# Performance work log

Hardware: AMD Instinct MI355X
Metric: run time of the kernel (lower is better)

The kernel has to match this reference:

```python
import jax, jax.numpy as jnp
import numpy as np

B, N_HIS, GRAPH_DIM, EMB, N_PRE = 32, 12, 307, 32, 12
DAY_STAMPS, WEEK_STATES = 288, 7
HID = EMB * N_PRE  # 384
STD, MEAN = 50.0, 60.0
LN_EPS = 1e-3  # keras LayerNormalization default epsilon


def setup_inputs() -> dict:
    key = jax.random.key(0)
    ks = jax.random.split(key, 32)
    gn = lambda k, shape, s: (jax.random.normal(k, shape, jnp.float32) * s)
    # inputs: [B, 1+n_his, 2+graph_dim]; row 0 carries (week, date) ids, rows 1: carry data
    x_data = gn(ks[0], (B, N_HIS, GRAPH_DIM), 1.0)
    week = jax.random.randint(ks[1], (B,), 0, WEEK_STATES)
    date = jax.random.randint(ks[2], (B,), 0, DAY_STAMPS)
    inputs = jnp.zeros((B, 1 + N_HIS, 2 + GRAPH_DIM), jnp.float32)
    inputs = inputs.at[:, 0, 0].set(week.astype(jnp.float32))
    inputs = inputs.at[:, 0, 1].set(date.astype(jnp.float32))
    inputs = inputs.at[:, 1:, 2:].set(x_data)
    d = {
        'inputs': inputs,
        'conv_w': gn(ks[3], (EMB,), 0.5),        # 1x1 Conv2D on 1 input channel
        'conv_b': gn(ks[4], (EMB,), 0.1),
        'dws': gn(ks[5], (DAY_STAMPS, N_HIS, EMB, EMB, N_HIS), (2.0 / (EMB * N_HIS)) ** 0.5),
        'dbs': gn(ks[6], (DAY_STAMPS, GRAPH_DIM, EMB, N_HIS), 0.02),
        'ln_gamma': jnp.ones((N_HIS,), jnp.float32),
        'ln_beta': jnp.zeros((N_HIS,), jnp.float32),
        'tge2tg': gn(ks[7], (GRAPH_DIM, EMB, GRAPH_DIM), (1.0 / (GRAPH_DIM * EMB)) ** 0.5),
        'gte2gt': gn(ks[8], (N_HIS, EMB, N_HIS), (1.0 / (N_HIS * EMB)) ** 0.5),
        'fully_w': gn(ks[9], (2 * N_HIS, N_PRE), (1.0 / (2 * N_HIS)) ** 0.5),
    }
    shapes = [(N_HIS, HID), (HID,), (HID, HID), (HID,), (HID, HID), (HID,), (HID, N_PRE), (N_PRE,)]
    names = ['w0', 'b0', 'w1', 'b1', 'w2', 'b2', 'w3', 'b3']
    ki = 10
    for pre in ('se_', 'te_'):
        for nm, sh in zip(names, shapes):
            s = 0.0 if nm.startswith('b') else (2.0 / sum(sh)) ** 0.5
            d[pre + nm] = gn(ks[ki], sh, s) if s > 0 else jnp.zeros(sh, jnp.float32)
            ki += 1
    return d


def _mlp(x, w0, b0, w1, b1, w2, b2, w3, b3):
    # MLP(layer_num=2): Dense(relu) -> Dense -> Dense(relu) -> Dense
    x = jax.nn.relu(x @ w0 + b0) @ w1 + b1
    x = jax.nn.relu(x @ w2 + b2) @ w3 + b3
    return x


def _forward(inputs, conv_w, conv_b, dws, dbs, ln_gamma, ln_beta,
             se_p, te_p, tge2tg, gte2gt, fully_w, date):
    x3 = inputs[:, 1:, 2:]                         # [B, t, g]
    xe = x3[..., None] * conv_w + conv_b           # 1x1 conv -> [B, t, g, e]
    xe = jnp.transpose(xe, (0, 2, 3, 1))           # [B, g, e, t]  ('bget')
    # talinear (dilation=False, week_flag=True): gather per-date weights, batched einsum
    dw = dws[date]                                 # [B, t, e, e, t']  ('bteij')
    db = dbs[date]                                 # [B, g, e, t']
    x = jnp.einsum('bget,bteij->bgij', xe, dw) + db
    # LayerNorm over last axis (n_his), keras default eps=1e-3
    m = jnp.mean(x, axis=-1, keepdims=True)
    v = jnp.var(x, axis=-1, keepdims=True)
    x = (x - m) * jax.lax.rsqrt(v + LN_EPS) * ln_gamma + ln_beta
    x = jnp.where(x >= 0, x, 0.3 * x)              # LeakyReLU(alpha=0.3); dropout inactive at inference
    xe2 = jnp.transpose(x, (0, 3, 1, 2))           # [B, t, g, e]
    tge = xe2
    gte = xe2.reshape(xe2.shape[0], GRAPH_DIM, N_HIS, EMB)  # faithful raw reshape (not transpose)
    x3t = jnp.transpose(x3, (0, 2, 1))             # [B, g, t]
    x1 = _mlp(x3t, *se_p)                          # [B, g, n_pre]
    x2 = _mlp(x3t, *te_p)
    tg = jnp.einsum('gev,btge->btv', tge2tg, tge)  # [B, t, g]
    tg2gt = jnp.transpose(tg, (0, 2, 1))           # [B, g, t]
    gt1 = (tg2gt + x1) * jax.nn.sigmoid(tg2gt)
    gt = jnp.einsum('teo,bgte->bgo', gte2gt, gte)  # [B, g, t]
    gt2 = (gt + x2) * jax.nn.sigmoid(gt)
    out = jnp.concatenate([gt1, gt2], axis=-1) @ fully_w  # [B, g, n_pre]
    out = jnp.transpose(out, (0, 2, 1)) * STD + MEAN      # z_inverse
    return out


def reference(inputs, conv_w, conv_b, dws, dbs, ln_gamma, ln_beta,
              se_w0, se_b0, se_w1, se_b1, se_w2, se_b2, se_w3, se_b3,
              te_w0, te_b0, te_w1, te_b1, te_w2, te_b2, te_w3, te_b3,
              tge2tg, gte2gt, fully_w):
    date = inputs[:, 0, 1].astype(jnp.int32)
    se_p = (se_w0, se_b0, se_w1, se_b1, se_w2, se_b2, se_w3, se_b3)
    te_p = (te_w0, te_b0, te_w1, te_b1, te_w2, te_b2, te_w3, te_b3)
    return _forward(inputs, conv_w, conv_b, dws, dbs, ln_gamma, ln_beta,
                    se_p, te_p, tge2tg, gte2gt, fully_w, date)
```

## Files before the change

kernel.cpp:

```cpp
#include <hip/hip_runtime.h>
#include <hip/hip_bf16.h>

#define NB   32
#define GDIM 307
#define IN_ROW 309
#define IN_B  (13*309)
#define NROWS (NB*GDIM)
#define MPAD  9856

typedef __attribute__((ext_vector_type(8))) short bf16x8;
typedef __attribute__((ext_vector_type(4))) float f32x4;

__device__ __forceinline__ void async_copy16(const void* g, void* l) {
  __builtin_amdgcn_global_load_lds(
      (const __attribute__((address_space(1))) void*)g,
      (__attribute__((address_space(3))) void*)l, 16, 0, 0);
}

__device__ __forceinline__ void mgemm_body(
    const __hip_bfloat16* __restrict__ A, int ldA,
    const __hip_bfloat16* __restrict__ Bt, int ldB,
    const float* bias, void* C, int ldC, long Czoff,
    int M, int N, int kt0, int kt1, int act, int outbf,
    char* smem, int m0, int n0) {
  const int tid = threadIdx.x;
  const int w = tid >> 6, lane = tid & 63;
  f32x4 acc[4][2];
  #pragma unroll
  for (int i=0;i<4;i++)
    #pragma unroll
    for (int j=0;j<2;j++) acc[i][j] = (f32x4){0.f,0.f,0.f,0.f};
  const int wm = (w>>1)*64, wn = (w&1)*32;
  const int l15 = lane & 15, lhi = lane >> 4;

  for (int kt = kt0; kt < kt1; ++kt) {
    const int k0 = kt*64;
    #pragma unroll
    for (int i=0;i<4;i++) {
      int c = w*256 + i*64 + lane;
      int row = c >> 3, j = c & 7;
      int jg = j ^ (row & 7);
      async_copy16(A + (size_t)(m0+row)*ldA + k0 + jg*8, smem + (w*256 + i*64)*16);
    }
    #pragma unroll
    for (int i=0;i<2;i++) {
      int c = w*128 + i*64 + lane;
      int row = c >> 3, j = c & 7;
      int jg = j ^ (row & 7);
      async_copy16(Bt + (size_t)(n0+row)*ldB + k0 + jg*8, smem + 16384 + (w*128 + i*64)*16);
    }
    __syncthreads();
    #pragma unroll
    for (int kk=0;kk<2;kk++) {
      bf16x8 af[4], bfr[2];
      #pragma unroll
      for (int fi=0; fi<4; fi++) {
        int row = wm + fi*16 + l15;
        af[fi] = *(const bf16x8*)(smem + row*128 + (((kk<<2)+lhi) ^ (row&7))*16);
      }
      #pragma unroll
      for (int fj=0; fj<2; fj++) {
        int n = wn + fj*16 + l15;
        bfr[fj] = *(const bf16x8*)(smem + 16384 + n*128 + (((kk<<2)+lhi) ^ (n&7))*16);
      }
      #pragma unroll
      for (int fi=0;fi<4;fi++)
        #pragma unroll
        for (int fj=0;fj<2;fj++)
          acc[fi][fj] = __builtin_amdgcn_mfma_f32_16x16x32_bf16(af[fi], bfr[fj], acc[fi][fj], 0, 0, 0);
    }
    __syncthreads();
  }

  #pragma unroll
  for (int fi=0;fi<4;fi++) {
    int row0 = m0 + wm + fi*16 + lhi*4;
    #pragma unroll
    for (int fj=0;fj<2;fj++) {
      int col = n0 + wn + fj*16 + l15;
      if (col < N) {
        float bv = bias ? bias[col] : 0.f;
        #pragma unroll
        for (int r=0;r<4;r++) {
          int row = row0 + r;
          if (row < M) {
            float v = acc[fi][fj][r] + bv;
            if (act) v = fmaxf(v, 0.f);
            if (outbf)
              ((__hip_bfloat16*)C)[(size_t)row*ldC + col] = __float2bfloat16(v);
            else
              ((float*)C + Czoff)[(size_t)row*ldC + col] = v;
          }
        }
      }
    }
  }
}

__global__ __launch_bounds__(256) void k_f1(
    const float* __restrict__ inp, const float* __restrict__ dws,
    const float* __restrict__ cw, const float* __restrict__ cb,
    float* __restrict__ A_pre, float* __restrict__ Cp,
    const float* se1, const float* se2, const float* te1, const float* te2,
    const float* se3, const float* te3, const float* g2g, const float* tgw,
    __hip_bfloat16* Wse1, __hip_bfloat16* Wse2, __hip_bfloat16* Wte1, __hip_bfloat16* Wte2,
    __hip_bfloat16* Wse3, __hip_bfloat16* Wte3, __hip_bfloat16* Wgt, __hip_bfloat16* Wtg,
    const float* se0, const float* seb0, const float* te0, const float* teb0,
    __hip_bfloat16* __restrict__ hA_se, __hip_bfloat16* __restrict__ hA_te) {
  __shared__ char smem[23040];
  int bid = blockIdx.x, tid = threadIdx.x;
  if (bid < 932) {
    float (*t)[65] = (float(*)[65])smem;
    const float* src; __hip_bfloat16* dst; int sK, sN, dR, ldD, bx, by;
    if (bid < 144) {
      int q = bid / 36, s = bid % 36; bx = s % 6; by = s / 6;
      src = q==0?se1 : q==1?se2 : q==2?te1 : te2;
      dst = q==0?Wse1: q==1?Wse2: q==2?Wte1: Wte2;
      sK = 384; sN = 384; dR = 384; ldD = 384;
    } else if (bid < 162) {
      int q = (bid-144)/6, s = (bid-144)%6; bx = s; by = 0;
      src = q==0?se3:q==1?te3:g2g;
      dst = q==0?Wse3:q==1?Wte3:Wgt;
      sK = 384; sN = 12; dR = 64; ldD = 384;
    } else {
      int s = bid - 162; bx = s % 154; by = s / 154;
      src = tgw; dst = Wtg; sK = 9824; sN = 307; dR = 320; ldD = 9856;
    }
    int k0 = bx*64, n0 = by*64;
    int tx = tid & 63, ty = tid >> 6;
    for (int r = ty; r < 64; r += 4) {
      int k = k0 + r, n = n0 + tx;
      t[r][tx] = (k < sK && n < sN) ? src[(size_t)k*sN + n] : 0.f;
    }
    __syncthreads();
    for (int r = ty; r < 64; r += 4) {
      int n = n0 + r, k = k0 + tx;
      if (n < dR && k < ldD) dst[(size_t)n*ldD + k] = __float2bfloat16(t[tx][r]);
    }
  } else if (bid < 1240) {
    int idx = bid - 932;
    int z = idx / 154, mt = idx - z*154;
    int r0 = mt*64;
    const float* w0 = z ? te0 : se0;
    const float* b0 = z ? teb0 : seb0;
    __hip_bfloat16* H = z ? hA_te : hA_se;
    float* sw = (float*)smem;
    float* sb = sw + 4608;
    float* sx = sb + 384;
    for (int i = tid; i < 4608; i += 256) sw[i] = w0[i];
    for (int i = tid; i < 384; i += 256) sb[i] = b0[i];
    for (int v = tid; v < 768; v += 256) {
      int r = v / 12, t = v - r*12;
      int row = r0 + r;
      float xv = 0.f;
      if (row < NROWS) {
        int b = row / GDIM, g = row - b*GDIM;
        xv = inp[b*IN_B + (1+t)*IN_ROW + 2 + g];
      }
      sx[v] = xv;
    }
    __syncthreads();
    for (int c = tid; c < 384; c += 256) {
      float wv[12];
      #pragma unroll
      for (int t = 0; t < 12; t++) wv[t] = sw[t*384 + c];
      float bv = sb[c];
      for (int r = 0; r < 64; r++) {
        int row = r0 + r;
        if (row >= NROWS) break;
        float acc = bv;
        #pragma unroll
        for (int t = 0; t < 12; t++) acc += sx[r*12+t] * wv[t];
        H[(size_t)row*384 + c] = __float2bfloat16(fmaxf(acc, 0.f));
      }
    }
  } else {
    int idx = bid - 1240;
    int b = idx / 12, t = idx - b*12;
    float* scw = (float*)smem;
    float* scb = scw + 32;
    if (tid < 32) { scw[tid] = cw[tid]; scb[tid] = cb[tid]; }
    __syncthreads();
    int date = (int)inp[b*IN_B + 1];
    const float* dw = dws + (size_t)date * 147456 + t*12288;
    for (int r = tid; r < 384; r += 256) {
      float sA = 0.f, sC = 0.f;
      #pragma unroll
      for (int e = 0; e < 32; e++) {
        float v = dw[e*384 + r];
        sA += scw[e] * v;
        sC += scb[e] * v;
      }
      A_pre[(b*12 + t)*384 + r] = sA;
      Cp[(b*12 + t)*384 + r]    = sC;
    }
  }
}

__global__ __launch_bounds__(256) void k_f2(
    const __hip_bfloat16* __restrict__ hA_se, const __hip_bfloat16* __restrict__ hA_te,
    const __hip_bfloat16* __restrict__ Wse1, const __hip_bfloat16* __restrict__ Wte1,
    const float* __restrict__ seb1, const float* __restrict__ teb1,
    __hip_bfloat16* __restrict__ hB_se, __hip_bfloat16* __restrict__ hB_te,
    const float* __restrict__ inp, const float* __restrict__ dbs,
    const float* __restrict__ A_pre, const float* __restrict__ Cp,
    const float* __restrict__ gamma, const float* __restrict__ beta,
    __hip_bfloat16* __restrict__ xlnT, __hip_bfloat16* __restrict__ xg) {
  __shared__ char smem[32640];
  int bid = blockIdx.x, tid = threadIdx.x;
  if (bid < 924) {
    int z = bid / 462, rem = bid - z*462;
    int n0 = (rem % 6)*64, m0 = (rem / 6)*128;
    mgemm_body(z ? hA_te : hA_se, 384, z ? Wte1 : Wse1, 384,
               z ? teb1 : seb1, z ? hB_te : hB_se, 384, 0,
               NROWS, 384, 0, 6, 0, 1, smem, m0, n0);
  } else {
    int idx = bid - 924;
    int b = idx / 39, gc = idx - b*39;
    int g0 = gc*8, ng = min(8, GDIM - g0);
    float* sA  = (float*)smem;
    float* sxb = sA + 4608;
    float* sCs = sxb + 3072;
    float* sx3 = sCs + 384;
    int date = (int)inp[b*IN_B + 1];
    for (int v = tid; v < 4608; v += 256) sA[v] = A_pre[b*4608 + v];
    for (int e = tid; e < 384; e += 256) {
      float s = 0.f;
      #pragma unroll
      for (int t = 0; t < 12; t++) s += Cp[b*4608 + t*384 + e];
      sCs[e] = s;
    }
    if (tid < ng*12) {
      int gl = tid / 12, t = tid - gl*12;
      sx3[tid] = inp[b*IN_B + (1+t)*IN_ROW + 2 + g0 + gl];
    }
    if (gc == 38) {
      for (int v = tid; v < 384; v += 256) {
        int j = v >> 5, c = v & 31;
        xlnT[(size_t)(b*12+j)*9856 + 9824 + c] = __float2bfloat16(0.f);
      }
    }
    __syncthreads();
    for (int o = tid; o < ng*384; o += 256) {
      int gl = o / 384, e = o - gl*384;
      float acc = sCs[e] + dbs[(size_t)date*117888 + (g0+gl)*384 + e];
      #pragma unroll
      for (int t = 0; t < 12; t++) acc += sx3[gl*12+t] * sA[t*384 + e];
      sxb[gl*384 + e] = acc;
    }
    __syncthreads();
    if (tid < ng*32) {
      int gl = tid >> 5, i = tid & 31;
      const float* xb = sxb + gl*384 + i*12;
      float m = 0.f;
      #pragma unroll
      for (int q = 0; q < 12; q++) m += xb[q];
      m *= (1.f/12.f);
      float v = 0.f;
      #pragma unroll
      for (int q = 0; q < 12; q++) { float d = xb[q] - m; v += d*d; }
      v *= (1.f/12.f);
      float rs = rsqrtf(v + 1e-3f);
      int g = g0 + gl;
      #pragma unroll
      for (int j = 0; j < 12; j++) {
        float y = (xb[j] - m) * rs * gamma[j] + beta[j];
        y = (y >= 0.f) ? y : 0.3f*y;
        __hip_bfloat16 yb = __float2bfloat16(y);
        xlnT[(size_t)(b*12 + j)*9856 + g*32 + i] = yb;
        int q2 = j*GDIM + g;
        int gq = q2 / 12, tq = q2 - gq*12;
        xg[(size_t)(b*GDIM + gq)*384 + tq*32 + i] = yb;
      }
    }
  }
}

__global__ __launch_bounds__(256) void k_f3(
    const __hip_bfloat16* __restrict__ hB_se, const __hip_bfloat16* __restrict__ hB_te,
    const __hip_bfloat16* __restrict__ Wse2, const __hip_bfloat16* __restrict__ Wte2,
    const float* __restrict__ seb2, const float* __restrict__ teb2,
    __hip_bfloat16* __restrict__ hA_se, __hip_bfloat16* __restrict__ hA_te,
    const __hip_bfloat16* __restrict__ xlnT, const __hip_bfloat16* __restrict__ Wtg,
    float* __restrict__ tgp,
    const __hip_bfloat16* __restrict__ xg, const __hip_bfloat16* __restrict__ Wgt,
    float* __restrict__ gtv) {
  __shared__ char smem[24576];
  int bid = blockIdx.x;
  if (bid < 924) {
    int z = bid / 462, rem = bid - z*462;
    int n0 = (rem % 6)*64, m0 = (rem / 6)*128;
    mgemm_body(z ? hB_te : hB_se, 384, z ? Wte2 : Wse2, 384,
               z ? teb2 : seb2, z ? hA_te : hA_se, 384, 0,
               NROWS, 384, 0, 6, 1, 1, smem, m0, n0);
  } else if (bid < 1164) {
    int idx = bid - 924;
    int z = idx / 15, rem = idx - z*15;
    int n0 = (rem % 5)*64, m0 = (rem / 5)*128;
    int kt0 = z*10, kt1 = min(154, kt0 + 10);
    mgemm_body(xlnT, 9856, Wtg, 9856, nullptr, tgp, 320, (long)z*122880,
               384, 320, kt0, kt1, 0, 0, smem, m0, n0);
  } else {
    int m0 = (bid - 1164)*128;
    mgemm_body(xg, 384, Wgt, 384, nullptr, gtv, 12, 0,
               NROWS, 12, 0, 6, 0, 0, smem, m0, 0);
  }
}

__global__ __launch_bounds__(256) void k_f4(
    const __hip_bfloat16* __restrict__ hA_se, const __hip_bfloat16* __restrict__ hA_te,
    const __hip_bfloat16* __restrict__ Wse3, const __hip_bfloat16* __restrict__ Wte3,
    const float* __restrict__ seb3, const float* __restrict__ teb3,
    float* __restrict__ x1, float* __restrict__ x2,
    const float* __restrict__ tgp, float* __restrict__ tgv) {
  __shared__ char smem[24576];
  int bid = blockIdx.x;
  if (bid < 154) {
    int z = bid / 77, m0 = (bid - z*77)*128;
    mgemm_body(z ? hA_te : hA_se, 384, z ? Wte3 : Wse3, 384,
               z ? teb3 : seb3, z ? x2 : x1, 12, 0,
               NROWS, 12, 0, 6, 0, 0, smem, m0, 0);
  } else {
    int base = (bid - 154) * 1024;
    #pragma unroll
    for (int q = 0; q < 4; q++) {
      int gid = base + q*256 + threadIdx.x;
      float s = 0.f;
      #pragma unroll
      for (int z = 0; z < 16; z++) s += tgp[(size_t)z*122880 + gid];
      tgv[gid] = s;
    }
  }
}

__global__ __launch_bounds__(256) void k_final(const float* __restrict__ tgv,
    const float* __restrict__ gt, const float* __restrict__ x1,
    const float* __restrict__ x2, const float* __restrict__ fw,
    float* __restrict__ out) {
  __shared__ float w[288];
  for (int idx = threadIdx.x; idx < 288; idx += 256) w[idx] = fw[idx];
  __syncthreads();
  int gid = blockIdx.x*256 + threadIdx.x;
  if (gid >= NROWS) return;
  int b = gid / GDIM, g = gid - b*GDIM;
  float g1[12], g2[12];
  #pragma unroll
  for (int n = 0; n < 12; n++) {
    float tv  = tgv[(size_t)(b*12+n)*320 + g];
    float x1v = x1[(size_t)gid*12 + n];
    float gv  = gt[(size_t)gid*12 + n];
    float x2v = x2[(size_t)gid*12 + n];
    float s1 = 1.f/(1.f + __expf(-tv));
    float s2 = 1.f/(1.f + __expf(-gv));
    g1[n] = (tv + x1v)*s1;
    g2[n] = (gv + x2v)*s2;
  }
  #pragma unroll
  for (int o = 0; o < 12; o++) {
    float acc = 0.f;
    #pragma unroll
    for (int n = 0; n < 12; n++)
      acc += g1[n]*w[n*12+o] + g2[n]*w[(12+n)*12+o];
    out[(size_t)(b*12+o)*GDIM + g] = acc*50.f + 60.f;
  }
}

extern "C" void kernel_launch(void* const* d_in, const int* in_sizes, int n_in,
                              void* d_out, int out_size, void* d_ws, size_t ws_size,
                              hipStream_t stream) {
  const float* inp    = (const float*)d_in[0];
  const float* cw     = (const float*)d_in[1];
  const float* cb     = (const float*)d_in[2];
  const float* dws    = (const float*)d_in[3];
  const float* dbs    = (const float*)d_in[4];
  const float* ln_g   = (const float*)d_in[5];
  const float* ln_b   = (const float*)d_in[6];
  const float* tge2tg = (const float*)d_in[7];
  const float* gte2gt = (const float*)d_in[8];
  const float* fullyw = (const float*)d_in[9];
  const float* se[8];
  const float* te[8];
  for (int i = 0; i < 8; i++) { se[i] = (const float*)d_in[10+i]; te[i] = (const float*)d_in[18+i]; }
  float* out = (float*)d_out;

  char* base = (char*)d_ws;
  size_t off = 0;
  auto alloc = [&](size_t bytes) { char* r = base + off; off += (bytes + 255) & ~(size_t)255; return r; };
  float* A_pre = (float*)alloc(147456*4);
  float* Cp    = (float*)alloc(147456*4);
  float* x1    = (float*)alloc(117888*4);
  float* x2    = (float*)alloc(117888*4);
  float* gtv   = (float*)alloc(117888*4);
  float* tgv   = (float*)alloc(122880*4);
  float* tgp   = (float*)alloc((size_t)16*122880*4);
  __hip_bfloat16* hA_se = (__hip_bfloat16*)alloc((size_t)MPAD*384*2);
  __hip_bfloat16* hA_te = (__hip_bfloat16*)alloc((size_t)MPAD*384*2);
  __hip_bfloat16* hB_se = (__hip_bfloat16*)alloc((size_t)MPAD*384*2);
  __hip_bfloat16* hB_te = (__hip_bfloat16*)alloc((size_t)MPAD*384*2);
  __hip_bfloat16* xlnT  = (__hip_bfloat16*)alloc((size_t)384*9856*2);
  __hip_bfloat16* xg    = (__hip_bfloat16*)alloc((size_t)MPAD*384*2);
  __hip_bfloat16* Wse1 = (__hip_bfloat16*)alloc(147456*2);
  __hip_bfloat16* Wse2 = (__hip_bfloat16*)alloc(147456*2);
  __hip_bfloat16* Wte1 = (__hip_bfloat16*)alloc(147456*2);
  __hip_bfloat16* Wte2 = (__hip_bfloat16*)alloc(147456*2);
  __hip_bfloat16* Wse3 = (__hip_bfloat16*)alloc(24576*2);
  __hip_bfloat16* Wte3 = (__hip_bfloat16*)alloc(24576*2);
  __hip_bfloat16* Wgt  = (__hip_bfloat16*)alloc(24576*2);
  __hip_bfloat16* Wtg  = (__hip_bfloat16*)alloc((size_t)320*9856*2);

  k_f1<<<1624, 256, 0, stream>>>(inp, dws, cw, cb, A_pre, Cp,
      se[2], se[4], te[2], te[4], se[6], te[6], gte2gt, tge2tg,
      Wse1, Wse2, Wte1, Wte2, Wse3, Wte3, Wgt, Wtg,
      se[0], se[1], te[0], te[1], hA_se, hA_te);

  k_f2<<<2172, 256, 0, stream>>>(hA_se, hA_te, Wse1, Wte1, se[3], te[3],
      hB_se, hB_te, inp, dbs, A_pre, Cp, ln_g, ln_b, xlnT, xg);

  k_f3<<<1241, 256, 0, stream>>>(hB_se, hB_te, Wse2, Wte2, se[5], te[5],
      hA_se, hA_te, xlnT, Wtg, tgp, xg, Wgt, gtv);

  k_f4<<<274, 256, 0, stream>>>(hA_se, hA_te, Wse3, Wte3, se[7], te[7], x1, x2, tgp, tgv);

  k_final<<<39, 256, 0, stream>>>(tgv, gtv, x1, x2, fullyw, out);
}
```

Measured before the change: 112.3 us.

## Fuse final MLP layer, split-K reduction and output gating into one kernel

Merges the last MLP GEMM, the split-K reduction of the tg partials and the final gating/projection into a single 512-thread kernel. The x1/x2 results now stay in LDS and never round-trip through global memory. The tg split-K count drops from 16 to 8 so each block covers more K, and block orderings are changed so the long-running tg GEMM and Wtg transpose blocks are dispatched first. This removes one launch and several intermediate buffers, but leaves only 77 blocks for the final stage and each thread sums 8 partials inline.

```diff
diff --git a/kernel.cpp b/kernel.cpp
--- a/kernel.cpp
+++ b/kernel.cpp
@@ -11,6 +11,15 @@
 typedef __attribute__((ext_vector_type(8))) short bf16x8;
 typedef __attribute__((ext_vector_type(4))) float f32x4;
 
+struct KP {
+  const float *inp,*dws,*cw,*cb,*dbs,*ln_g,*ln_b,*g2g,*tgw,*fw;
+  const float *se0,*seb0,*sew1,*seb1,*sew2,*seb2,*sew3,*seb3;
+  const float *te0,*teb0,*tew1,*teb1,*tew2,*teb2,*tew3,*teb3;
+  float *A_pre,*Cp,*gtv,*tgp,*out;
+  __hip_bfloat16 *hA_se,*hA_te,*hB_se,*hB_te,*xlnT,*xg;
+  __hip_bfloat16 *Wse1,*Wse2,*Wte1,*Wte2,*Wse3,*Wte3,*Wgt,*Wtg;
+};
+
 __device__ __forceinline__ void async_copy16(const void* g, void* l) {
   __builtin_amdgcn_global_load_lds(
       (const __attribute__((address_space(1))) void*)g,
@@ -21,9 +30,8 @@
     const __hip_bfloat16* __restrict__ A, int ldA,
     const __hip_bfloat16* __restrict__ Bt, int ldB,
     const float* bias, void* C, int ldC, long Czoff,
-    int M, int N, int kt0, int kt1, int act, int outbf,
-    char* smem, int m0, int n0) {
-  const int tid = threadIdx.x;
+    int M, int N, int kt0, int kt1, int act, int mode,
+    char* smem, int m0, int n0, float* ldsOut, int tid) {
   const int w = tid >> 6, lane = tid & 63;
   f32x4 acc[4][2];
   #pragma unroll
@@ -72,6 +80,22 @@
     __syncthreads();
   }
 
+  if (mode == 2) {
+    #pragma unroll
+    for (int fi=0;fi<4;fi++) {
+      int rl0 = wm + fi*16 + lhi*4;
+      #pragma unroll
+      for (int fj=0;fj<2;fj++) {
+        int col = wn + fj*16 + l15;
+        if (col < N) {
+          float bv = bias ? bias[col] : 0.f;
+          #pragma unroll
+          for (int r=0;r<4;r++) ldsOut[(rl0+r)*13 + col] = acc[fi][fj][r] + bv;
+        }
+      }
+    }
+    return;
+  }
   #pragma unroll
   for (int fi=0;fi<4;fi++) {
     int row0 = m0 + wm + fi*16 + lhi*4;
@@ -86,7 +110,7 @@
           if (row < M) {
             float v = acc[fi][fj][r] + bv;
             if (act) v = fmaxf(v, 0.f);
-            if (outbf)
+            if (mode == 1)
               ((__hip_bfloat16*)C)[(size_t)row*ldC + col] = __float2bfloat16(v);
             else
               ((float*)C + Czoff)[(size_t)row*ldC + col] = v;
@@ -97,34 +121,45 @@
   }
 }
 
-__global__ __launch_bounds__(256) void k_f1(
-    const float* __restrict__ inp, const float* __restrict__ dws,
-    const float* __restrict__ cw, const float* __restrict__ cb,
-    float* __restrict__ A_pre, float* __restrict__ Cp,
-    const float* se1, const float* se2, const float* te1, const float* te2,
-    const float* se3, const float* te3, const float* g2g, const float* tgw,
-    __hip_bfloat16* Wse1, __hip_bfloat16* Wse2, __hip_bfloat16* Wte1, __hip_bfloat16* Wte2,
-    __hip_bfloat16* Wse3, __hip_bfloat16* Wte3, __hip_bfloat16* Wgt, __hip_bfloat16* Wtg,
-    const float* se0, const float* seb0, const float* te0, const float* teb0,
-    __hip_bfloat16* __restrict__ hA_se, __hip_bfloat16* __restrict__ hA_te) {
-  __shared__ char smem[23040];
+__global__ __launch_bounds__(256) void k_p1(KP P) {
+  __shared__ alignas(16) char smem[23040];
   int bid = blockIdx.x, tid = threadIdx.x;
-  if (bid < 932) {
+  if (bid < 384) {
+    int b = bid / 12, t = bid - b*12;
+    float* scw = (float*)smem;
+    float* scb = scw + 32;
+    if (tid < 32) { scw[tid] = P.cw[tid]; scb[tid] = P.cb[tid]; }
+    __syncthreads();
+    int date = (int)P.inp[b*IN_B + 1];
+    const float* dw = P.dws + (size_t)date * 147456 + t*12288;
+    for (int r = tid; r < 384; r += 256) {
+      float sA = 0.f, sC = 0.f;
+      #pragma unroll
+      for (int e = 0; e < 32; e++) {
+        float v = dw[e*384 + r];
+        sA += scw[e] * v;
+        sC += scb[e] * v;
+      }
+      P.A_pre[(b*12 + t)*384 + r] = sA;
+      P.Cp[(b*12 + t)*384 + r]    = sC;
+    }
+  } else if (bid < 1316) {
     float (*t)[65] = (float(*)[65])smem;
+    int s = bid - 384;
     const float* src; __hip_bfloat16* dst; int sK, sN, dR, ldD, bx, by;
-    if (bid < 144) {
-      int q = bid / 36, s = bid % 36; bx = s % 6; by = s / 6;
-      src = q==0?se1 : q==1?se2 : q==2?te1 : te2;
-      dst = q==0?Wse1: q==1?Wse2: q==2?Wte1: Wte2;
+    if (s < 770) {
+      bx = s % 154; by = s / 154;
+      src = P.tgw; dst = P.Wtg; sK = 9824; sN = 307; dR = 320; ldD = 9856;
+    } else if (s < 914) {
+      int q = (s-770) / 36, u = (s-770) % 36; bx = u % 6; by = u / 6;
+      src = q==0?P.sew1 : q==1?P.sew2 : q==2?P.tew1 : P.tew2;
+      dst = q==0?P.Wse1 : q==1?P.Wse2 : q==2?P.Wte1 : P.Wte2;
       sK = 384; sN = 384; dR = 384; ldD = 384;
-    } else if (bid < 162) {
-      int q = (bid-144)/6, s = (bid-144)%6; bx = s; by = 0;
-      src = q==0?se3:q==1?te3:g2g;
-      dst = q==0?Wse3:q==1?Wte3:Wgt;
+    } else {
+      int q = (s-914) / 6, u = (s-914) % 6; bx = u; by = 0;
+      src = q==0?P.sew3 : q==1?P.tew3 : P.g2g;
+      dst = q==0?P.Wse3 : q==1?P.Wte3 : P.Wgt;
       sK = 384; sN = 12; dR = 64; ldD = 384;
-    } else {
-      int s = bid - 162; bx = s % 154; by = s / 154;
-      src = tgw; dst = Wtg; sK = 9824; sN = 307; dR = 320; ldD = 9856;
     }
     int k0 = bx*64, n0 = by*64;
     int tx = tid & 63, ty = tid >> 6;
@@ -137,13 +172,13 @@
       int n = n0 + r, k = k0 + tx;
       if (n < dR && k < ldD) dst[(size_t)n*ldD + k] = __float2bfloat16(t[tx][r]);
     }
-  } else if (bid < 1240) {
-    int idx = bid - 932;
+  } else {
+    int idx = bid - 1316;
     int z = idx / 154, mt = idx - z*154;
     int r0 = mt*64;
-    const float* w0 = z ? te0 : se0;
-    const float* b0 = z ? teb0 : seb0;
-    __hip_bfloat16* H = z ? hA_te : hA_se;
+    const float* w0 = z ? P.te0 : P.se0;
+    const float* b0 = z ? P.teb0 : P.seb0;
+    __hip_bfloat16* H = z ? P.hA_te : P.hA_se;
     float* sw = (float*)smem;
     float* sb = sw + 4608;
     float* sx = sb + 384;
@@ -155,7 +190,7 @@
       float xv = 0.f;
       if (row < NROWS) {
         int b = row / GDIM, g = row - b*GDIM;
-        xv = inp[b*IN_B + (1+t)*IN_ROW + 2 + g];
+        xv = P.inp[b*IN_B + (1+t)*IN_ROW + 2 + g];
       }
       sx[v] = xv;
     }
@@ -174,46 +209,17 @@
         H[(size_t)row*384 + c] = __float2bfloat16(fmaxf(acc, 0.f));
       }
     }
-  } else {
-    int idx = bid - 1240;
-    int b = idx / 12, t = idx - b*12;
-    float* scw = (float*)smem;
-    float* scb = scw + 32;
-    if (tid < 32) { scw[tid] = cw[tid]; scb[tid] = cb[tid]; }
-    __syncthreads();
-    int date = (int)inp[b*IN_B + 1];
-    const float* dw = dws + (size_t)date * 147456 + t*12288;
-    for (int r = tid; r < 384; r += 256) {
-      float sA = 0.f, sC = 0.f;
-      #pragma unroll
-      for (int e = 0; e < 32; e++) {
-        float v = dw[e*384 + r];
-        sA += scw[e] * v;
-        sC += scb[e] * v;
-      }
-      A_pre[(b*12 + t)*384 + r] = sA;
-      Cp[(b*12 + t)*384 + r]    = sC;
-    }
-  }
-}
-
-__global__ __launch_bounds__(256) void k_f2(
-    const __hip_bfloat16* __restrict__ hA_se, const __hip_bfloat16* __restrict__ hA_te,
-    const __hip_bfloat16* __restrict__ Wse1, const __hip_bfloat16* __restrict__ Wte1,
-    const float* __restrict__ seb1, const float* __restrict__ teb1,
-    __hip_bfloat16* __restrict__ hB_se, __hip_bfloat16* __restrict__ hB_te,
-    const float* __restrict__ inp, const float* __restrict__ dbs,
-    const float* __restrict__ A_pre, const float* __restrict__ Cp,
-    const float* __restrict__ gamma, const float* __restrict__ beta,
-    __hip_bfloat16* __restrict__ xlnT, __hip_bfloat16* __restrict__ xg) {
-  __shared__ char smem[32640];
+  }
+}
+
+__global__ __launch_bounds__(256) void k_p2(KP P) {
+  __shared__ alignas(16) char smem[32640];
   int bid = blockIdx.x, tid = threadIdx.x;
   if (bid < 924) {
     int z = bid / 462, rem = bid - z*462;
-    int n0 = (rem % 6)*64, m0 = (rem / 6)*128;
-    mgemm_body(z ? hA_te : hA_se, 384, z ? Wte1 : Wse1, 384,
-               z ? teb1 : seb1, z ? hB_te : hB_se, 384, 0,
-               NROWS, 384, 0, 6, 0, 1, smem, m0, n0);
+    mgemm_body(z ? P.hA_te : P.hA_se, 384, z ? P.Wte1 : P.Wse1, 384,
+               z ? P.teb1 : P.seb1, z ? P.hB_te : P.hB_se, 384, 0,
+               NROWS, 384, 0, 6, 0, 1, smem, (rem/6)*128, (rem%6)*64, nullptr, tid);
   } else {
     int idx = bid - 924;
     int b = idx / 39, gc = idx - b*39;
@@ -222,28 +228,28 @@
     float* sxb = sA + 4608;
     float* sCs = sxb + 3072;
     float* sx3 = sCs + 384;
-    int date = (int)inp[b*IN_B + 1];
-    for (int v = tid; v < 4608; v += 256) sA[v] = A_pre[b*4608 + v];
+    int date = (int)P.inp[b*IN_B + 1];
+    for (int v = tid; v < 4608; v += 256) sA[v] = P.A_pre[b*4608 + v];
     for (int e = tid; e < 384; e += 256) {
       float s = 0.f;
       #pragma unroll
-      for (int t = 0; t < 12; t++) s += Cp[b*4608 + t*384 + e];
+      for (int t = 0; t < 12; t++) s += P.Cp[b*4608 + t*384 + e];
       sCs[e] = s;
     }
     if (tid < ng*12) {
       int gl = tid / 12, t = tid - gl*12;
-      sx3[tid] = inp[b*IN_B + (1+t)*IN_ROW + 2 + g0 + gl];
+      sx3[tid] = P.inp[b*IN_B + (1+t)*IN_ROW + 2 + g0 + gl];
     }
     if (gc == 38) {
       for (int v = tid; v < 384; v += 256) {
         int j = v >> 5, c = v & 31;
-        xlnT[(size_t)(b*12+j)*9856 + 9824 + c] = __float2bfloat16(0.f);
+        P.xlnT[(size_t)(b*12+j)*9856 + 9824 + c] = __float2bfloat16(0.f);
       }
     }
     __syncthreads();
     for (int o = tid; o < ng*384; o += 256) {
       int gl = o / 384, e = o - gl*384;
-      float acc = sCs[e] + dbs[(size_t)date*117888 + (g0+gl)*384 + e];
+      float acc = sCs[e] + P.dbs[(size_t)date*117888 + (g0+gl)*384 + e];
       #pragma unroll
       for (int t = 0; t < 12; t++) acc += sx3[gl*12+t] * sA[t*384 + e];
       sxb[gl*384 + e] = acc;
@@ -264,162 +270,131 @@
       int g = g0 + gl;
       #pragma unroll
       for (int j = 0; j < 12; j++) {
-        float y = (xb[j] - m) * rs * gamma[j] + beta[j];
+        float y = (xb[j] - m) * rs * P.ln_g[j] + P.ln_b[j];
         y = (y >= 0.f) ? y : 0.3f*y;
         __hip_bfloat16 yb = __float2bfloat16(y);
-        xlnT[(size_t)(b*12 + j)*9856 + g*32 + i] = yb;
+        P.xlnT[(size_t)(b*12 + j)*9856 + g*32 + i] = yb;
         int q2 = j*GDIM + g;
         int gq = q2 / 12, tq = q2 - gq*12;
-        xg[(size_t)(b*GDIM + gq)*384 + tq*32 + i] = yb;
-      }
-    }
-  }
-}
-
-__global__ __launch_bounds__(256) void k_f3(
-    const __hip_bfloat16* __restrict__ hB_se, const __hip_bfloat16* __restrict__ hB_te,
-    const __hip_bfloat16* __restrict__ Wse2, const __hip_bfloat16* __restrict__ Wte2,
-    const float* __restrict__ seb2, const float* __restrict__ teb2,
-    __hip_bfloat16* __restrict__ hA_se, __hip_bfloat16* __restrict__ hA_te,
-    const __hip_bfloat16* __restrict__ xlnT, const __hip_bfloat16* __restrict__ Wtg,
-    float* __restrict__ tgp,
-    const __hip_bfloat16* __restrict__ xg, const __hip_bfloat16* __restrict__ Wgt,
-    float* __restrict__ gtv) {
-  __shared__ char smem[24576];
-  int bid = blockIdx.x;
-  if (bid < 924) {
-    int z = bid / 462, rem = bid - z*462;
-    int n0 = (rem % 6)*64, m0 = (rem / 6)*128;
-    mgemm_body(z ? hB_te : hB_se, 384, z ? Wte2 : Wse2, 384,
-               z ? teb2 : seb2, z ? hA_te : hA_se, 384, 0,
-               NROWS, 384, 0, 6, 1, 1, smem, m0, n0);
-  } else if (bid < 1164) {
-    int idx = bid - 924;
-    int z = idx / 15, rem = idx - z*15;
-    int n0 = (rem % 5)*64, m0 = (rem / 5)*128;
-    int kt0 = z*10, kt1 = min(154, kt0 + 10);
-    mgemm_body(xlnT, 9856, Wtg, 9856, nullptr, tgp, 320, (long)z*122880,
-               384, 320, kt0, kt1, 0, 0, smem, m0, n0);
+        P.xg[(size_t)(b*GDIM + gq)*384 + tq*32 + i] = yb;
+      }
+    }
+  }
+}
+
+__global__ __launch_bounds__(256) void k_p3(KP P) {
+  __shared__ alignas(16) char smem[24576];
+  int bid = blockIdx.x, tid = threadIdx.x;
+  if (bid < 120) {
+    int z = bid / 15, rem = bid - z*15;
+    int kt0 = z*20, kt1 = min(154, kt0 + 20);
+    mgemm_body(P.xlnT, 9856, P.Wtg, 9856, nullptr, P.tgp, 320, (long)z*122880,
+               384, 320, kt0, kt1, 0, 0, smem, (rem/5)*128, (rem%5)*64, nullptr, tid);
+  } else if (bid < 1044) {
+    int idx = bid - 120;
+    int z = idx / 462, rem = idx - z*462;
+    mgemm_body(z ? P.hB_te : P.hB_se, 384, z ? P.Wte2 : P.Wse2, 384,
+               z ? P.teb2 : P.seb2, z ? P.hA_te : P.hA_se, 384, 0,
+               NROWS, 384, 0, 6, 1, 1, smem, (rem/6)*128, (rem%6)*64, nullptr, tid);
   } else {
-    int m0 = (bid - 1164)*128;
-    mgemm_body(xg, 384, Wgt, 384, nullptr, gtv, 12, 0,
-               NROWS, 12, 0, 6, 0, 0, smem, m0, 0);
-  }
-}
-
-__global__ __launch_bounds__(256) void k_f4(
-    const __hip_bfloat16* __restrict__ hA_se, const __hip_bfloat16* __restrict__ hA_te,
-    const __hip_bfloat16* __restrict__ Wse3, const __hip_bfloat16* __restrict__ Wte3,
-    const float* __restrict__ seb3, const float* __restrict__ teb3,
-    float* __restrict__ x1, float* __restrict__ x2,
-    const float* __restrict__ tgp, float* __restrict__ tgv) {
-  __shared__ char smem[24576];
-  int bid = blockIdx.x;
-  if (bid < 154) {
-    int z = bid / 77, m0 = (bid - z*77)*128;
-    mgemm_body(z ? hA_te : hA_se, 384, z ? Wte3 : Wse3, 384,
-               z ? teb3 : seb3, z ? x2 : x1, 12, 0,
-               NROWS, 12, 0, 6, 0, 0, smem, m0, 0);
-  } else {
-    int base = (bid - 154) * 1024;
-    #pragma unroll
-    for (int q = 0; q < 4; q++) {
-      int gid = base + q*256 + threadIdx.x;
-      float s = 0.f;
-      #pragma unroll
-      for (int z = 0; z < 16; z++) s += tgp[(size_t)z*122880 + gid];
-      tgv[gid] = s;
-    }
-  }
-}
-
-__global__ __launch_bounds__(256) void k_final(const float* __restrict__ tgv,
-    const float* __restrict__ gt, const float* __restrict__ x1,
-    const float* __restrict__ x2, const float* __restrict__ fw,
-    float* __restrict__ out) {
-  __shared__ float w[288];
-  for (int idx = threadIdx.x; idx < 288; idx += 256) w[idx] = fw[idx];
+    int m0 = (bid - 1044)*128;
+    mgemm_body(P.xg, 384, P.Wgt, 384, nullptr, P.gtv, 12, 0,
+               NROWS, 12, 0, 6, 0, 0, smem, m0, 0, nullptr, tid);
+  }
+}
+
+__global__ __launch_bounds__(512) void k_p4(KP P) {
+  __shared__ alignas(16) char smem[63616];
+  float* x1s = (float*)(smem + 49152);
+  float* x2s = x1s + 1664;
+  float* fws = x2s + 1664;
+  int tid = threadIdx.x;
+  int half = tid >> 8, lt = tid & 255;
+  int r0 = blockIdx.x * 128;
+  for (int i = tid; i < 288; i += 512) fws[i] = P.fw[i];
+  mgemm_body(half ? P.hA_te : P.hA_se, 384, half ? P.Wte3 : P.Wse3, 384,
+             half ? P.teb3 : P.seb3, nullptr, 0, 0, NROWS, 12, 0, 6, 0, 2,
+             smem + half*24576, r0, 0, half ? x2s : x1s, lt);
   __syncthreads();
-  int gid = blockIdx.x*256 + threadIdx.x;
-  if (gid >= NROWS) return;
-  int b = gid / GDIM, g = gid - b*GDIM;
-  float g1[12], g2[12];
-  #pragma unroll
-  for (int n = 0; n < 12; n++) {
-    float tv  = tgv[(size_t)(b*12+n)*320 + g];
-    float x1v = x1[(size_t)gid*12 + n];
-    float gv  = gt[(size_t)gid*12 + n];
-    float x2v = x2[(size_t)gid*12 + n];
-    float s1 = 1.f/(1.f + __expf(-tv));
-    float s2 = 1.f/(1.f + __expf(-gv));
-    g1[n] = (tv + x1v)*s1;
-    g2[n] = (gv + x2v)*s2;
-  }
-  #pragma unroll
-  for (int o = 0; o < 12; o++) {
-    float acc = 0.f;
-    #pragma unroll
-    for (int n = 0; n < 12; n++)
-      acc += g1[n]*w[n*12+o] + g2[n]*w[(12+n)*12+o];
-    out[(size_t)(b*12+o)*GDIM + g] = acc*50.f + 60.f;
+  if (tid < 128) {
+    int row = r0 + tid;
+    if (row < NROWS) {
+      int b = row / GDIM, g = row - b*GDIM;
+      float g1[12], g2[12];
+      #pragma unroll
+      for (int n = 0; n < 12; n++) {
+        float tv = 0.f;
+        #pragma unroll
+        for (int z = 0; z < 8; z++) tv += P.tgp[(size_t)z*122880 + (b*12+n)*320 + g];
+        float gv  = P.gtv[(size_t)row*12 + n];
+        float x1v = x1s[tid*13 + n];
+        float x2v = x2s[tid*13 + n];
+        float s1 = 1.f/(1.f + __expf(-tv));
+        float s2 = 1.f/(1.f + __expf(-gv));
+        g1[n] = (tv + x1v)*s1;
+        g2[n] = (gv + x2v)*s2;
+      }
+      #pragma unroll
+      for (int o = 0; o < 12; o++) {
+        float a = 0.f;
+        #pragma unroll
+        for (int n = 0; n < 12; n++)
+          a += g1[n]*fws[n*12+o] + g2[n]*fws[(12+n)*12+o];
+        P.out[(size_t)(b*12+o)*GDIM + g] = a*50.f + 60.f;
+      }
+    }
   }
 }
 
 extern "C" void kernel_launch(void* const* d_in, const int* in_sizes, int n_in,
                               void* d_out, int out_size, void* d_ws, size_t ws_size,
                               hipStream_t stream) {
-  const float* inp    = (const float*)d_in[0];
-  const float* cw     = (const float*)d_in[1];
-  const float* cb     = (const float*)d_in[2];
-  const float* dws    = (const float*)d_in[3];
-  const float* dbs    = (const float*)d_in[4];
-  const float* ln_g   = (const float*)d_in[5];
-  const float* ln_b   = (const float*)d_in[6];
-  const float* tge2tg = (const float*)d_in[7];
-  const float* gte2gt = (const float*)d_in[8];
-  const float* fullyw = (const float*)d_in[9];
   const float* se[8];
   const float* te[8];
   for (int i = 0; i < 8; i++) { se[i] = (const float*)d_in[10+i]; te[i] = (const float*)d_in[18+i]; }
-  float* out = (float*)d_out;
 
   char* base = (char*)d_ws;
   size_t off = 0;
   auto alloc = [&](size_t bytes) { char* r = base + off; off += (bytes + 255) & ~(size_t)255; return r; };
-  float* A_pre = (float*)alloc(147456*4);
-  float* Cp    = (float*)alloc(147456*4);
-  float* x1    = (float*)alloc(117888*4);
-  float* x2    = (float*)alloc(117888*4);
-  float* gtv   = (float*)alloc(117888*4);
-  float* tgv   = (float*)alloc(122880*4);
-  float* tgp   = (float*)alloc((size_t)16*122880*4);
-  __hip_bfloat16* hA_se = (__hip_bfloat16*)alloc((size_t)MPAD*384*2);
-  __hip_bfloat16* hA_te = (__hip_bfloat16*)alloc((size_t)MPAD*384*2);
-  __hip_bfloat16* hB_se = (__hip_bfloat16*)alloc((size_t)MPAD*384*2);
-  __hip_bfloat16* hB_te = (__hip_bfloat16*)alloc((size_t)MPAD*384*2);
-  __hip_bfloat16* xlnT  = (__hip_bfloat16*)alloc((size_t)384*9856*2);
-  __hip_bfloat16* xg    = (__hip_bfloat16*)alloc((size_t)MPAD*384*2);
-  __hip_bfloat16* Wse1 = (__hip_bfloat16*)alloc(147456*2);
-  __hip_bfloat16* Wse2 = (__hip_bfloat16*)alloc(147456*2);
-  __hip_bfloat16* Wte1 = (__hip_bfloat16*)alloc(147456*2);
-  __hip_bfloat16* Wte2 = (__hip_bfloat16*)alloc(147456*2);
-  __hip_bfloat16* Wse3 = (__hip_bfloat16*)alloc(24576*2);
-  __hip_bfloat16* Wte3 = (__hip_bfloat16*)alloc(24576*2);
-  __hip_bfloat16* Wgt  = (__hip_bfloat16*)alloc(24576*2);
-  __hip_bfloat16* Wtg  = (__hip_bfloat16*)alloc((size_t)320*9856*2);
-
-  k_f1<<<1624, 256, 0, stream>>>(inp, dws, cw, cb, A_pre, Cp,
-      se[2], se[4], te[2], te[4], se[6], te[6], gte2gt, tge2tg,
-      Wse1, Wse2, Wte1, Wte2, Wse3, Wte3, Wgt, Wtg,
-      se[0], se[1], te[0], te[1], hA_se, hA_te);
-
-  k_f2<<<2172, 256, 0, stream>>>(hA_se, hA_te, Wse1, Wte1, se[3], te[3],
-      hB_se, hB_te, inp, dbs, A_pre, Cp, ln_g, ln_b, xlnT, xg);
-
-  k_f3<<<1241, 256, 0, stream>>>(hB_se, hB_te, Wse2, Wte2, se[5], te[5],
-      hA_se, hA_te, xlnT, Wtg, tgp, xg, Wgt, gtv);
-
-  k_f4<<<274, 256, 0, stream>>>(hA_se, hA_te, Wse3, Wte3, se[7], te[7], x1, x2, tgp, tgv);
-
-  k_final<<<39, 256, 0, stream>>>(tgv, gtv, x1, x2, fullyw, out);
-}
+
+  KP P;
+  P.inp  = (const float*)d_in[0];
+  P.cw   = (const float*)d_in[1];
+  P.cb   = (const float*)d_in[2];
+  P.dws  = (const float*)d_in[3];
+  P.dbs  = (const float*)d_in[4];
+  P.ln_g = (const float*)d_in[5];
+  P.ln_b = (const float*)d_in[6];
+  P.tgw  = (const float*)d_in[7];
+  P.g2g  = (const float*)d_in[8];
+  P.fw   = (const float*)d_in[9];
+  P.se0 = se[0]; P.seb0 = se[1]; P.sew1 = se[2]; P.seb1 = se[3];
+  P.sew2 = se[4]; P.seb2 = se[5]; P.sew3 = se[6]; P.seb3 = se[7];
+  P.te0 = te[0]; P.teb0 = te[1]; P.tew1 = te[2]; P.teb1 = te[3];
+  P.tew2 = te[4]; P.teb2 = te[5]; P.tew3 = te[6]; P.teb3 = te[7];
+  P.out = (float*)d_out;
+
+  P.A_pre = (float*)alloc(147456*4);
+  P.Cp    = (float*)alloc(147456*4);
+  P.gtv   = (float*)alloc(117888*4);
+  P.tgp   = (float*)alloc((size_t)8*122880*4);
+  P.hA_se = (__hip_bfloat16*)alloc((size_t)MPAD*384*2);
+  P.hA_te = (__hip_bfloat16*)alloc((size_t)MPAD*384*2);
+  P.hB_se = (__hip_bfloat16*)alloc((size_t)MPAD*384*2);
+  P.hB_te = (__hip_bfloat16*)alloc((size_t)MPAD*384*2);
+  P.xlnT  = (__hip_bfloat16*)alloc((size_t)384*9856*2);
+  P.xg    = (__hip_bfloat16*)alloc((size_t)MPAD*384*2);
+  P.Wse1  = (__hip_bfloat16*)alloc(147456*2);
+  P.Wse2  = (__hip_bfloat16*)alloc(147456*2);
+  P.Wte1  = (__hip_bfloat16*)alloc(147456*2);
+  P.Wte2  = (__hip_bfloat16*)alloc(147456*2);
+  P.Wse3  = (__hip_bfloat16*)alloc(24576*2);
+  P.Wte3  = (__hip_bfloat16*)alloc(24576*2);
+  P.Wgt   = (__hip_bfloat16*)alloc(24576*2);
+  P.Wtg   = (__hip_bfloat16*)alloc((size_t)320*9856*2);
+
+  k_p1<<<1624, 256, 0, stream>>>(P);
+  k_p2<<<2172, 256, 0, stream>>>(P);
+  k_p3<<<1121, 256, 0, stream>>>(P);
+  k_p4<<<77, 512, 0, stream>>>(P);
+}
```

Result: slower. 131.5 us (+17.1%).

## Move weight transposes not needed by f2 GEMM into k_f2 to shorten k_f1

Applied to the files above, without the earlier changes.

k_f1 now only transposes the first-layer MLP weights it feeds to k_f2, plus the date-weight precompute and the first MLP layer. The large tge2tg transpose and the second/third-layer weight transposes move into k_f2 as extra blocks running alongside its GEMM and layernorm blocks. The date-precompute blocks are reordered to run first in k_f1. This shortens the critical path by overlapping independent preprocessing with later compute, at the cost of a larger, more heterogeneous k_f2 grid.

```diff
diff --git a/kernel.cpp b/kernel.cpp
--- a/kernel.cpp
+++ b/kernel.cpp
@@ -97,48 +97,53 @@
   }
 }
 
+__device__ __forceinline__ void tr_tile(const float* src, __hip_bfloat16* dst,
+    int sK, int sN, int dR, int ldD, int bx, int by, char* smem, int tid) {
+  float (*t)[65] = (float(*)[65])smem;
+  int k0 = bx*64, n0 = by*64;
+  int tx = tid & 63, ty = tid >> 6;
+  for (int r = ty; r < 64; r += 4) {
+    int k = k0 + r, n = n0 + tx;
+    t[r][tx] = (k < sK && n < sN) ? src[(size_t)k*sN + n] : 0.f;
+  }
+  __syncthreads();
+  for (int r = ty; r < 64; r += 4) {
+    int n = n0 + r, k = k0 + tx;
+    if (n < dR && k < ldD) dst[(size_t)n*ldD + k] = __float2bfloat16(t[tx][r]);
+  }
+}
+
 __global__ __launch_bounds__(256) void k_f1(
     const float* __restrict__ inp, const float* __restrict__ dws,
     const float* __restrict__ cw, const float* __restrict__ cb,
     float* __restrict__ A_pre, float* __restrict__ Cp,
-    const float* se1, const float* se2, const float* te1, const float* te2,
-    const float* se3, const float* te3, const float* g2g, const float* tgw,
-    __hip_bfloat16* Wse1, __hip_bfloat16* Wse2, __hip_bfloat16* Wte1, __hip_bfloat16* Wte2,
-    __hip_bfloat16* Wse3, __hip_bfloat16* Wte3, __hip_bfloat16* Wgt, __hip_bfloat16* Wtg,
+    const float* se1, const float* te1,
+    __hip_bfloat16* Wse1, __hip_bfloat16* Wte1,
     const float* se0, const float* seb0, const float* te0, const float* teb0,
     __hip_bfloat16* __restrict__ hA_se, __hip_bfloat16* __restrict__ hA_te) {
-  __shared__ char smem[23040];
+  __shared__ alignas(16) char smem[23040];
   int bid = blockIdx.x, tid = threadIdx.x;
-  if (bid < 932) {
-    float (*t)[65] = (float(*)[65])smem;
-    const float* src; __hip_bfloat16* dst; int sK, sN, dR, ldD, bx, by;
-    if (bid < 144) {
-      int q = bid / 36, s = bid % 36; bx = s % 6; by = s / 6;
-      src = q==0?se1 : q==1?se2 : q==2?te1 : te2;
-      dst = q==0?Wse1: q==1?Wse2: q==2?Wte1: Wte2;
-      sK = 384; sN = 384; dR = 384; ldD = 384;
-    } else if (bid < 162) {
-      int q = (bid-144)/6, s = (bid-144)%6; bx = s; by = 0;
-      src = q==0?se3:q==1?te3:g2g;
-      dst = q==0?Wse3:q==1?Wte3:Wgt;
-      sK = 384; sN = 12; dR = 64; ldD = 384;
-    } else {
-      int s = bid - 162; bx = s % 154; by = s / 154;
-      src = tgw; dst = Wtg; sK = 9824; sN = 307; dR = 320; ldD = 9856;
-    }
-    int k0 = bx*64, n0 = by*64;
-    int tx = tid & 63, ty = tid >> 6;
-    for (int r = ty; r < 64; r += 4) {
-      int k = k0 + r, n = n0 + tx;
-      t[r][tx] = (k < sK && n < sN) ? src[(size_t)k*sN + n] : 0.f;
-    }
-    __syncthreads();
-    for (int r = ty; r < 64; r += 4) {
-      int n = n0 + r, k = k0 + tx;
-      if (n < dR && k < ldD) dst[(size_t)n*ldD + k] = __float2bfloat16(t[tx][r]);
-    }
-  } else if (bid < 1240) {
-    int idx = bid - 932;
+  if (bid < 384) {
+    int b = bid / 12, t = bid - b*12;
+    float* scw = (float*)smem;
+    float* scb = scw + 32;
+    if (tid < 32) { scw[tid] = cw[tid]; scb[tid] = cb[tid]; }
+    __syncthreads();
+    int date = (int)inp[b*IN_B + 1];
+    const float* dw = dws + (size_t)date * 147456 + t*12288;
+    for (int r = tid; r < 384; r += 256) {
+      float sA = 0.f, sC = 0.f;
+      #pragma unroll
+      for (int e = 0; e < 32; e++) {
+        float v = dw[e*384 + r];
+        sA += scw[e] * v;
+        sC += scb[e] * v;
+      }
+      A_pre[(b*12 + t)*384 + r] = sA;
+      Cp[(b*12 + t)*384 + r]    = sC;
+    }
+  } else if (bid < 692) {
+    int idx = bid - 384;
     int z = idx / 154, mt = idx - z*154;
     int r0 = mt*64;
     const float* w0 = z ? te0 : se0;
@@ -175,25 +180,9 @@
       }
     }
   } else {
-    int idx = bid - 1240;
-    int b = idx / 12, t = idx - b*12;
-    float* scw = (float*)smem;
-    float* scb = scw + 32;
-    if (tid < 32) { scw[tid] = cw[tid]; scb[tid] = cb[tid]; }
-    __syncthreads();
-    int date = (int)inp[b*IN_B + 1];
-    const float* dw = dws + (size_t)date * 147456 + t*12288;
-    for (int r = tid; r < 384; r += 256) {
-      float sA = 0.f, sC = 0.f;
-      #pragma unroll
-      for (int e = 0; e < 32; e++) {
-        float v = dw[e*384 + r];
-        sA += scw[e] * v;
-        sC += scb[e] * v;
-      }
-      A_pre[(b*12 + t)*384 + r] = sA;
-      Cp[(b*12 + t)*384 + r]    = sC;
-    }
+    int s = bid - 692;
+    int q = s / 36, u = s % 36;
+    tr_tile(q ? te1 : se1, q ? Wte1 : Wse1, 384, 384, 384, 384, u % 6, u / 6, smem, tid);
   }
 }
 
@@ -205,17 +194,33 @@
     const float* __restrict__ inp, const float* __restrict__ dbs,
     const float* __restrict__ A_pre, const float* __restrict__ Cp,
     const float* __restrict__ gamma, const float* __restrict__ beta,
-    __hip_bfloat16* __restrict__ xlnT, __hip_bfloat16* __restrict__ xg) {
-  __shared__ char smem[32640];
+    __hip_bfloat16* __restrict__ xlnT, __hip_bfloat16* __restrict__ xg,
+    const float* se2, const float* te2, const float* se3, const float* te3,
+    const float* g2g, const float* tgw,
+    __hip_bfloat16* Wse2, __hip_bfloat16* Wte2, __hip_bfloat16* Wse3,
+    __hip_bfloat16* Wte3, __hip_bfloat16* Wgt, __hip_bfloat16* Wtg) {
+  __shared__ alignas(16) char smem[32640];
   int bid = blockIdx.x, tid = threadIdx.x;
   if (bid < 924) {
     int z = bid / 462, rem = bid - z*462;
-    int n0 = (rem % 6)*64, m0 = (rem / 6)*128;
     mgemm_body(z ? hA_te : hA_se, 384, z ? Wte1 : Wse1, 384,
                z ? teb1 : seb1, z ? hB_te : hB_se, 384, 0,
-               NROWS, 384, 0, 6, 0, 1, smem, m0, n0);
+               NROWS, 384, 0, 6, 0, 1, smem, (rem/6)*128, (rem%6)*64);
+  } else if (bid < 1784) {
+    int s = bid - 924;
+    if (s < 770) {
+      tr_tile(tgw, Wtg, 9824, 307, 320, 9856, s % 154, s / 154, smem, tid);
+    } else if (s < 842) {
+      int q = (s-770) / 36, u = (s-770) % 36;
+      tr_tile(q ? te2 : se2, q ? Wte2 : Wse2, 384, 384, 384, 384, u % 6, u / 6, smem, tid);
+    } else {
+      int q = (s-842) / 6, u = (s-842) % 6;
+      const float* src = q==0?se3 : q==1?te3 : g2g;
+      __hip_bfloat16* dst = q==0?Wse3 : q==1?Wte3 : Wgt;
+      tr_tile(src, dst, 384, 12, 64, 384, u, 0, smem, tid);
+    }
   } else {
-    int idx = bid - 924;
+    int idx = bid - 1784;
     int b = idx / 39, gc = idx - b*39;
     int g0 = gc*8, ng = min(8, GDIM - g0);
     float* sA  = (float*)smem;
@@ -285,14 +290,13 @@
     float* __restrict__ tgp,
     const __hip_bfloat16* __restrict__ xg, const __hip_bfloat16* __restrict__ Wgt,
     float* __restrict__ gtv) {
-  __shared__ char smem[24576];
+  __shared__ alignas(16) char smem[24576];
   int bid = blockIdx.x;
   if (bid < 924) {
     int z = bid / 462, rem = bid - z*462;
-    int n0 = (rem % 6)*64, m0 = (rem / 6)*128;
     mgemm_body(z ? hB_te : hB_se, 384, z ? Wte2 : Wse2, 384,
                z ? teb2 : seb2, z ? hA_te : hA_se, 384, 0,
-               NROWS, 384, 0, 6, 1, 1, smem, m0, n0);
+               NROWS, 384, 0, 6, 1, 1, smem, (rem/6)*128, (rem%6)*64);
   } else if (bid < 1164) {
     int idx = bid - 924;
     int z = idx / 15, rem = idx - z*15;
@@ -313,7 +317,7 @@
     const float* __restrict__ seb3, const float* __restrict__ teb3,
     float* __restrict__ x1, float* __restrict__ x2,
     const float* __restrict__ tgp, float* __restrict__ tgv) {
-  __shared__ char smem[24576];
+  __shared__ alignas(16) char smem[24576];
   int bid = blockIdx.x;
   if (bid < 154) {
     int z = bid / 77, m0 = (bid - z*77)*128;
@@ -408,13 +412,14 @@
   __hip_bfloat16* Wgt  = (__hip_bfloat16*)alloc(24576*2);
   __hip_bfloat16* Wtg  = (__hip_bfloat16*)alloc((size_t)320*9856*2);
 
-  k_f1<<<1624, 256, 0, stream>>>(inp, dws, cw, cb, A_pre, Cp,
-      se[2], se[4], te[2], te[4], se[6], te[6], gte2gt, tge2tg,
-      Wse1, Wse2, Wte1, Wte2, Wse3, Wte3, Wgt, Wtg,
+  k_f1<<<764, 256, 0, stream>>>(inp, dws, cw, cb, A_pre, Cp,
+      se[2], te[2], Wse1, Wte1,
       se[0], se[1], te[0], te[1], hA_se, hA_te);
 
-  k_f2<<<2172, 256, 0, stream>>>(hA_se, hA_te, Wse1, Wte1, se[3], te[3],
-      hB_se, hB_te, inp, dbs, A_pre, Cp, ln_g, ln_b, xlnT, xg);
+  k_f2<<<3032, 256, 0, stream>>>(hA_se, hA_te, Wse1, Wte1, se[3], te[3],
+      hB_se, hB_te, inp, dbs, A_pre, Cp, ln_g, ln_b, xlnT, xg,
+      se[4], te[4], se[6], te[6], gte2gt, tge2tg,
+      Wse2, Wte2, Wse3, Wte3, Wgt, Wtg);
 
   k_f3<<<1241, 256, 0, stream>>>(hB_se, hB_te, Wse2, Wte2, se[5], te[5],
       hA_se, hA_te, xlnT, Wtg, tgp, xg, Wgt, gtv);
```

Result: faster. 109.3 us (-2.7%).
